# Kernel tuning notes

Measured on AMD Instinct MI355X. Metric: run time of the kernel, lower is better.

The kernel has to match this reference:

```python
import jax, jax.numpy as jnp
import numpy as np

N_NODES = 50000
NUM_FEAT = 2000
HEADS = 8
HID = 8
NUM_CLASSES = 30
NUM_EDGES = 1_600_000
NEG_SLOPE = 0.2


def _segment_softmax(scores, seg, num_segments):
    # scores: [E, H], seg: [E] destination node ids
    m = jax.ops.segment_max(scores, seg, num_segments=num_segments)
    m = jnp.where(jnp.isfinite(m), m, 0.0)  # guard empty segments
    e = jnp.exp(scores - m[seg])
    s = jax.ops.segment_sum(e, seg, num_segments=num_segments)
    return e / (s[seg] + 1e-16)


def _gat_layer(x, src, dst, w, att_src, att_dst, bias, concat):
    # PyG GATConv (eval mode: dropout disabled). x: [N, F_in]
    n = x.shape[0]
    h_, c_ = att_src.shape
    h = (x @ w).reshape(n, h_, c_)                      # [N, H, C]
    a_src = (h * att_src[None]).sum(-1)                 # [N, H]
    a_dst = (h * att_dst[None]).sum(-1)                 # [N, H]
    alpha = jax.nn.leaky_relu(a_src[src] + a_dst[dst], NEG_SLOPE)  # [E, H]
    alpha = _segment_softmax(alpha, dst, n)             # per-dest softmax
    msg = h[src] * alpha[:, :, None]                    # [E, H, C]
    out = jax.ops.segment_sum(msg, dst, num_segments=n) # [N, H, C]
    out = out.reshape(n, h_ * c_) if concat else out.mean(axis=1)
    return out + bias, alpha


def _add_self_loops(edge_index, n):
    loops = jnp.arange(n, dtype=edge_index.dtype)
    src = jnp.concatenate([edge_index[0], loops])
    dst = jnp.concatenate([edge_index[1], loops])
    return src, dst


def setup_inputs() -> dict:
    key = jax.random.key(0)
    ks = jax.random.split(key, 12)
    x = jax.random.normal(ks[0], (N_NODES, NUM_FEAT), jnp.float32)
    edge_index = jax.random.randint(ks[1], (2, NUM_EDGES), 0, N_NODES, jnp.int32)
    d1 = HEADS * HID
    w_res = jax.random.normal(ks[2], (NUM_FEAT, d1), jnp.float32) / np.sqrt(NUM_FEAT)
    b_res = jnp.zeros((d1,), jnp.float32)
    w1 = jax.random.normal(ks[3], (NUM_FEAT, d1), jnp.float32) / np.sqrt(NUM_FEAT)
    att_src1 = jax.random.normal(ks[4], (HEADS, HID), jnp.float32) * 0.1
    att_dst1 = jax.random.normal(ks[5], (HEADS, HID), jnp.float32) * 0.1
    b1 = jnp.zeros((d1,), jnp.float32)
    w2 = jax.random.normal(ks[6], (d1, NUM_CLASSES), jnp.float32) / np.sqrt(d1)
    att_src2 = jax.random.normal(ks[7], (1, NUM_CLASSES), jnp.float32) * 0.1
    att_dst2 = jax.random.normal(ks[8], (1, NUM_CLASSES), jnp.float32) * 0.1
    b2 = jnp.zeros((NUM_CLASSES,), jnp.float32)
    return {"x": x, "edge_index": edge_index, "w_res": w_res, "b_res": b_res,
            "w1": w1, "att_src1": att_src1, "att_dst1": att_dst1, "b1": b1,
            "w2": w2, "att_src2": att_src2, "att_dst2": att_dst2, "b2": b2}


def reference(x, edge_index, w_res, b_res, w1, att_src1, att_dst1, b1,
              w2, att_src2, att_dst2, b2):
    n = x.shape[0]
    src, dst = _add_self_loops(edge_index, n)
    res = x @ w_res + b_res                                   # residual branch
    h1, alpha1 = _gat_layer(x, src, dst, w1, att_src1, att_dst1, b1, concat=True)
    x1 = jax.nn.elu(h1 + res)                                 # dropout = identity (eval)
    h2, alpha2 = _gat_layer(x1, src, dst, w2, att_src2, att_dst2, b2, concat=False)
    x2 = jax.nn.elu(h2)
    return jax.nn.log_softmax(x2, axis=1), alpha1, alpha2
```

## Files before the change

kernel.cpp:

```cpp
#include <hip/hip_runtime.h>
#include <hip/hip_bf16.h>

#define N_NODES 50000
#define NUM_FEAT 2000
#define HEADS 8
#define HID 8
#define NUM_CLASSES 30
#define NUM_EDGES 1600000
#define E_TOTAL (NUM_EDGES + N_NODES)
#define E8 (E_TOTAL * 8)
#define KT32 64
#define KT64 32
#define ROWCAP 128
#define LOG2E 1.44269504f
#define SENT N_NODES
#define NEG_BIG -1.0e30f

typedef __attribute__((ext_vector_type(8))) short short8;
typedef __attribute__((ext_vector_type(4))) float f32x4;

__device__ __forceinline__ ushort f2bf(float f) {
  __hip_bfloat16 b = __float2bfloat16(f);
  return *reinterpret_cast<ushort*>(&b);
}

__device__ __forceinline__ float bf2f(ushort u) {
  unsigned int x = ((unsigned int)u) << 16;
  union { unsigned int i; float f; } c; c.i = x;
  return c.f;
}

__device__ __forceinline__ float lexp2(float sc) {
  return exp2f(fmaxf(sc, 0.2f * sc));
}

__device__ __forceinline__ short8 cvt8(float4 a, float4 b) {
  union { short8 v; ushort u[8]; } p;
  p.u[0] = f2bf(a.x); p.u[1] = f2bf(a.y); p.u[2] = f2bf(a.z); p.u[3] = f2bf(a.w);
  p.u[4] = f2bf(b.x); p.u[5] = f2bf(b.y); p.u[6] = f2bf(b.z); p.u[7] = f2bf(b.w);
  return p.v;
}

__global__ void k_prepB(const float* __restrict__ Wres, const float* __restrict__ W1,
                        ushort* __restrict__ Bp) {
  int i = blockIdx.x * 256 + threadIdx.x;
  if (i >= KT32 * 4 * 128) return;
  int col = i & 127;
  int kbase = (i >> 7) * 8;
  const float* W = (col < 64) ? Wres : W1;
  int c = col & 63;
  union { short8 v; ushort u[8]; } p;
#pragma unroll
  for (int j = 0; j < 8; ++j) {
    int k = kbase + j;
    p.u[j] = f2bf(k < NUM_FEAT ? W[(size_t)k * 64 + c] : 0.f);
  }
  *(short8*)&Bp[(size_t)i * 8] = p.v;
}

__global__ __launch_bounds__(256) void k_prefill(int* __restrict__ esrc) {
  int i = blockIdx.x * 256 + threadIdx.x;
  if (i >= N_NODES * ROWCAP / 4) return;
  *(int4*)&esrc[i * 4] = make_int4(SENT, SENT, SENT, SENT);
}

__global__ __launch_bounds__(256) void k_gemm_mfma(const float* __restrict__ X,
    const ushort* __restrict__ Bp, const float* __restrict__ brs,
    const float* __restrict__ b1, float* __restrict__ Hres,
    ushort* __restrict__ Hatt) {
  __shared__ ushort ldsB[2][8192];
  const int tid = threadIdx.x;
  const int lane = tid & 63, wid = tid >> 6;
  const int lg = lane >> 4, lr = lane & 15;
  const int m0 = blockIdx.x * 64;

  int rowg = m0 + wid * 16 + lr;
  rowg = rowg < N_NODES ? rowg : N_NODES - 1;
  const float* axp = X + (size_t)rowg * NUM_FEAT + lg * 8;
  const short8* bsrc = (const short8*)Bp;

  f32x4 acc[8] = {};
  float4 a[4], na[4];
  short8 gb[4];
  const float4 fz = make_float4(0.f, 0.f, 0.f, 0.f);

  auto loadA = [&](int t, float4* r) {
#pragma unroll
    for (int s = 0; s < 2; ++s) {
      int k0 = t * 64 + s * 32 + lg * 8;
      if (k0 < NUM_FEAT) {
        r[2 * s]     = *(const float4*)(axp + t * 64 + s * 32);
        r[2 * s + 1] = *(const float4*)(axp + t * 64 + s * 32 + 4);
      } else { r[2 * s] = fz; r[2 * s + 1] = fz; }
    }
  };
  auto loadB = [&](int t) {
#pragma unroll
    for (int q = 0; q < 4; ++q) gb[q] = bsrc[(size_t)t * 1024 + q * 256 + tid];
  };
  auto writeB = [&](int buf) {
#pragma unroll
    for (int q = 0; q < 4; ++q)
      *(short8*)&ldsB[buf][(size_t)(q * 256 + tid) * 8] = gb[q];
  };
  auto mfmaStep = [&](int cur, const float4* av) {
#pragma unroll
    for (int s = 0; s < 2; ++s) {
      short8 fb[8];
#pragma unroll
      for (int n = 0; n < 8; ++n)
        fb[n] = *(const short8*)&ldsB[cur][(size_t)(s * 512 + lg * 128 + n * 16 + lr) * 8];
      short8 fa = cvt8(av[2 * s], av[2 * s + 1]);
#pragma unroll
      for (int n = 0; n < 8; ++n)
        acc[n] = __builtin_amdgcn_mfma_f32_16x16x32_bf16(fa, fb[n], acc[n], 0, 0, 0);
    }
  };

  loadB(0);
  loadA(0, a);
  writeB(0);
  asm volatile("s_waitcnt lgkmcnt(0)" ::: "memory");
  __builtin_amdgcn_s_barrier();
  __builtin_amdgcn_sched_barrier(0);

  for (int t = 0; t < KT64 - 1; ++t) {
    const int cur = t & 1, nxt = cur ^ 1;
    loadB(t + 1);
    loadA(t + 1, na);
    mfmaStep(cur, a);
    writeB(nxt);
    asm volatile("s_waitcnt lgkmcnt(0)" ::: "memory");
    __builtin_amdgcn_s_barrier();
    __builtin_amdgcn_sched_barrier(0);
#pragma unroll
    for (int q = 0; q < 4; ++q) a[q] = na[q];
  }
  mfmaStep((KT64 - 1) & 1, a);

#pragma unroll
  for (int n = 0; n < 8; ++n) {
    int col = n * 16 + lr;
    if (col < 64) {
      float badd = brs[col] + b1[col];
#pragma unroll
      for (int i = 0; i < 4; ++i) {
        int row = m0 + wid * 16 + lg * 4 + i;
        if (row < N_NODES) Hres[(size_t)row * 64 + col] = acc[n][i] + badd;
      }
    } else {
#pragma unroll
      for (int i = 0; i < 4; ++i) {
        int row = m0 + wid * 16 + lg * 4 + i;
        if (row < N_NODES) Hatt[(size_t)row * 64 + (col - 64)] = f2bf(acc[n][i]);
      }
    }
  }
}

__global__ void k_fill_attn(const int* __restrict__ ei, int* __restrict__ cursor,
                            int* __restrict__ esrc, ushort* __restrict__ Hatt,
                            const float* __restrict__ att_src,
                            const float* __restrict__ att_dst,
                            float* __restrict__ a_src, float2* __restrict__ dinv1) {
  int i = blockIdx.x * 256 + threadIdx.x;
  if (i < N_NODES * HEADS) {
    int h = i & 7;
    const ushort* hp = &Hatt[(size_t)(i >> 3) * 64 + h * 8];
    float s = 0.f, d = 0.f;
#pragma unroll
    for (int c = 0; c < 8; ++c) {
      float v = bf2f(hp[c]);
      s = fmaf(v, att_src[h * 8 + c], s);
      d = fmaf(v, att_dst[h * 8 + c], d);
    }
    a_src[i] = s * LOG2E;
    dinv1[i] = make_float2(d * LOG2E, 0.f);
  }
  if (i < E_TOTAL) {
    int s, d;
    if (i < NUM_EDGES) { s = ei[i]; d = ei[NUM_EDGES + i]; }
    else { s = d = i - NUM_EDGES; }
    int pos = atomicAdd(&cursor[d], 1);
    esrc[(unsigned)(d * ROWCAP + pos)] = s;
  }
  if (i < 64) Hatt[(size_t)SENT * 64 + i] = 0;
  if (i >= 64 && i < 72) a_src[SENT * 8 + (i - 64)] = NEG_BIG;
}

__global__ __launch_bounds__(256) void k_layer1f(const int* __restrict__ esrc,
    const int* __restrict__ cursor,
    const float* __restrict__ Hres, const ushort* __restrict__ Hatt,
    const float* __restrict__ a_src, float2* __restrict__ dinv1,
    const float* __restrict__ w2, const float* __restrict__ att_src2,
    const float* __restrict__ att_dst2, ushort* __restrict__ h2b,
    float* __restrict__ a_src2, float2* __restrict__ dinv2) {
  __shared__ float w2s[64 * 30];
  __shared__ float xs[4][64];
  for (int i = threadIdx.x; i < 64 * 30; i += 256) w2s[i] = w2[i];
  if (blockIdx.x == 0) {
    if (threadIdx.x < 32) h2b[(unsigned)(SENT * 32 + threadIdx.x)] = 0;
    if (threadIdx.x == 32) a_src2[SENT] = NEG_BIG;
  }
  __syncthreads();
  int wave = threadIdx.x >> 6, lane = threadIdx.x & 63;
  int n = blockIdx.x * 4 + wave;
  if (n >= N_NODES) return;
  int hd = lane >> 3;
  float adn = dinv1[(unsigned)(n * 8 + hd)].x;
  int start = n * ROWCAP, end = start + ((cursor[n] + 7) & ~7);
  float denom = 0.f, msg = 0.f;
  for (int p = start; p < end; p += 8) {
    int4 v0 = *(const int4*)&esrc[p];
    int4 v1 = *(const int4*)&esrc[p + 4];
    int s8[8] = {v0.x, v0.y, v0.z, v0.w, v1.x, v1.y, v1.z, v1.w};
    float av[8];
    ushort hu[8];
#pragma unroll
    for (int i = 0; i < 8; ++i) {
      av[i] = a_src[(unsigned)(s8[i] * 8 + hd)];
      hu[i] = Hatt[(unsigned)(s8[i] * 64 + lane)];
    }
#pragma unroll
    for (int i = 0; i < 8; ++i) {
      float ev = lexp2(av[i] + adn);
      denom += ev;
      msg = fmaf(ev, bf2f(hu[i]), msg);
    }
  }
  float invd = 1.f / (denom + 1e-16f);
  float x1v = msg * invd + Hres[(unsigned)(n * 64 + lane)];
  x1v = x1v > 0.f ? x1v : __expf(x1v) - 1.f;
  if ((lane & 7) == 0) dinv1[(unsigned)(n * 8 + hd)].y = invd;

  xs[wave][lane] = x1v;
  float acc2 = 0.f;
  if (lane < 30) {
#pragma unroll 8
    for (int k = 0; k < 64; ++k) acc2 = fmaf(xs[wave][k], w2s[k * 30 + lane], acc2);
  }
  float as = (lane < 30) ? acc2 * att_src2[lane] : 0.f;
  float ad = (lane < 30) ? acc2 * att_dst2[lane] : 0.f;
  for (int off = 1; off < 64; off <<= 1) {
    as += __shfl_xor(as, off);
    ad += __shfl_xor(ad, off);
  }
  if (lane == 0) { a_src2[n] = as * LOG2E; dinv2[n] = make_float2(ad * LOG2E, 0.f); }
  if (lane < 32) h2b[(unsigned)(n * 32 + lane)] = (lane < 30) ? f2bf(acc2) : (ushort)0;
}

__global__ __launch_bounds__(256) void k_layer2(const int* __restrict__ esrc,
    const int* __restrict__ cursor,
    const ushort* __restrict__ h2b, const float* __restrict__ a_src2,
    float2* __restrict__ dinv2, const float* __restrict__ b2,
    float* __restrict__ out0) {
  int wave = threadIdx.x >> 6, lane = threadIdx.x & 63;
  int n = blockIdx.x * 4 + wave;
  if (n >= N_NODES) return;
  float adn = dinv2[n].x;
  int start = n * ROWCAP, end = start + ((cursor[n] + 7) & ~7);
  int half = lane >> 5, cls = lane & 31;
  float denom = 0.f, msg = 0.f;
  for (int p = start; p < end; p += 4) {
    int s0 = esrc[p + half];
    int s1 = esrc[p + 2 + half];
    float as0 = a_src2[(unsigned)s0], as1 = a_src2[(unsigned)s1];
    ushort hv0 = h2b[(unsigned)(s0 * 32 + cls)];
    ushort hv1 = h2b[(unsigned)(s1 * 32 + cls)];
    float ev0 = lexp2(as0 + adn);
    denom += ev0;
    msg = fmaf(ev0, bf2f(hv0), msg);
    float ev1 = lexp2(as1 + adn);
    denom += ev1;
    msg = fmaf(ev1, bf2f(hv1), msg);
  }
  denom += __shfl_xor(denom, 32);
  msg   += __shfl_xor(msg, 32);
  float invd = 1.f / (denom + 1e-16f);
  bool act = lane < 30;
  float o = act ? msg * invd + b2[lane] : 0.f;
  float x2 = o > 0.f ? o : __expf(o) - 1.f;
  float mv = act ? x2 : -1e30f;
  for (int off = 1; off < 64; off <<= 1) mv = fmaxf(mv, __shfl_xor(mv, off));
  float ex = act ? __expf(x2 - mv) : 0.f;
  for (int off = 1; off < 64; off <<= 1) ex += __shfl_xor(ex, off);
  if (act) out0[(size_t)n * 30 + lane] = x2 - mv - __logf(ex);
  if (lane == 0) dinv2[n].y = invd;
}

__global__ __launch_bounds__(256) void k_alpha(const int* __restrict__ ei,
    const float* __restrict__ a_src1, const float2* __restrict__ dinv1,
    const float* __restrict__ a_src2, const float2* __restrict__ dinv2,
    float* __restrict__ alpha1, float* __restrict__ alpha2) {
  int i = blockIdx.x * 256 + threadIdx.x;
  if (i >= E8) return;
  {
    int e = i >> 3, h = i & 7;
    int s, d;
    if (e < NUM_EDGES) { s = ei[e]; d = ei[NUM_EDGES + e]; }
    else { s = d = e - NUM_EDGES; }
    float2 di = dinv1[(unsigned)(d * 8 + h)];
    alpha1[i] = lexp2(a_src1[(unsigned)(s * 8 + h)] + di.x) * di.y;
  }
  if (i < E_TOTAL) {
    int s, d;
    if (i < NUM_EDGES) { s = ei[i]; d = ei[NUM_EDGES + i]; }
    else { s = d = i - NUM_EDGES; }
    float2 dj = dinv2[(unsigned)d];
    alpha2[i] = lexp2(a_src2[(unsigned)s] + dj.x) * dj.y;
  }
}

extern "C" void kernel_launch(void* const* d_in, const int* in_sizes, int n_in,
                              void* d_out, int out_size, void* d_ws, size_t ws_size,
                              hipStream_t stream) {
  const float* x        = (const float*)d_in[0];
  const int*   ei       = (const int*)d_in[1];
  const float* w_res    = (const float*)d_in[2];
  const float* b_res    = (const float*)d_in[3];
  const float* w1       = (const float*)d_in[4];
  const float* att_src1 = (const float*)d_in[5];
  const float* att_dst1 = (const float*)d_in[6];
  const float* b1       = (const float*)d_in[7];
  const float* w2       = (const float*)d_in[8];
  const float* att_src2 = (const float*)d_in[9];
  const float* att_dst2 = (const float*)d_in[10];
  const float* b2       = (const float*)d_in[11];

  float* ws = (float*)d_ws;
  float* Hres    = ws;
  float* a_src1  = Hres + (size_t)N_NODES * 64;
  float2* dinv1  = (float2*)(a_src1 + (size_t)(N_NODES + 1) * 8);
  float* a_src2  = (float*)(dinv1 + (size_t)N_NODES * 8);
  float2* dinv2  = (float2*)(a_src2 + N_NODES + 1);
  ushort* Hatt   = (ushort*)(dinv2 + N_NODES);
  ushort* h2b    = Hatt + (size_t)(N_NODES + 1) * 64;
  ushort* Bp     = h2b + (size_t)(N_NODES + 1) * 32 + 32;
  int*   cursor  = (int*)(Bp + (size_t)KT32 * 4096 + 64);

  float* out0   = (float*)d_out;
  float* alpha1 = out0 + (size_t)N_NODES * 30;
  float* alpha2 = alpha1 + (size_t)E8;
  int*   esrc   = (int*)alpha1;

  hipMemsetAsync(cursor, 0, N_NODES * sizeof(int), stream);

  k_prefill<<<(N_NODES * ROWCAP / 4 + 255) / 256, 256, 0, stream>>>(esrc);
  k_prepB<<<(KT32 * 4 * 128 + 255) / 256, 256, 0, stream>>>(w_res, w1, Bp);
  k_gemm_mfma<<<(N_NODES + 63) / 64, 256, 0, stream>>>(x, Bp, b_res, b1, Hres, Hatt);
  k_fill_attn<<<(E_TOTAL + 255) / 256, 256, 0, stream>>>(ei, cursor, esrc, Hatt,
                                                         att_src1, att_dst1,
                                                         a_src1, dinv1);
  k_layer1f<<<(N_NODES + 3) / 4, 256, 0, stream>>>(esrc, cursor, Hres, Hatt,
                                                   a_src1, dinv1, w2, att_src2,
                                                   att_dst2, h2b, a_src2, dinv2);
  k_layer2<<<(N_NODES + 3) / 4, 256, 0, stream>>>(esrc, cursor, h2b, a_src2,
                                                  dinv2, b2, out0);
  k_alpha<<<(E8 + 255) / 256, 256, 0, stream>>>(ei, a_src1, dinv1, a_src2, dinv2,
                                                alpha1, alpha2);
}
```

Measured before the change: 436.4 us.

## Load GEMM B tiles directly into LDS and fuse init kernels

The GEMM now stages the bf16 weight tiles with global_load_lds (direct global-to-LDS DMA) instead of loading into registers and writing to LDS, and waits on vmcnt rather than lgkmcnt before the barrier. This removes the register round-trip and the LDS store instructions from the main loop, which frees VGPRs and issue slots. Separately, the memset, the sentinel prefill and the weight-packing kernels are merged into one init kernel to cut launch overhead. The vmcnt(4) wait has to count outstanding loads correctly. If the compiler reorders the A loads and the DMA, the barrier could read stale LDS.

```diff
diff --git a/kernel.cpp b/kernel.cpp
--- a/kernel.cpp
+++ b/kernel.cpp
@@ -19,6 +19,13 @@
 typedef __attribute__((ext_vector_type(8))) short short8;
 typedef __attribute__((ext_vector_type(4))) float f32x4;
 
+typedef __attribute__((address_space(1))) const unsigned int gu32;
+typedef __attribute__((address_space(3))) unsigned int lu32;
+
+__device__ __forceinline__ void gload_lds16(const void* g, void* l) {
+  __builtin_amdgcn_global_load_lds((gu32*)g, (lu32*)l, 16, 0, 0);
+}
+
 __device__ __forceinline__ ushort f2bf(float f) {
   __hip_bfloat16 b = __float2bfloat16(f);
   return *reinterpret_cast<ushort*>(&b);
@@ -41,27 +48,27 @@
   return p.v;
 }
 
-__global__ void k_prepB(const float* __restrict__ Wres, const float* __restrict__ W1,
-                        ushort* __restrict__ Bp) {
+__global__ __launch_bounds__(256) void k_init(int* __restrict__ esrc,
+    const float* __restrict__ Wres, const float* __restrict__ W1,
+    ushort* __restrict__ Bp, int* __restrict__ cursor) {
   int i = blockIdx.x * 256 + threadIdx.x;
-  if (i >= KT32 * 4 * 128) return;
-  int col = i & 127;
-  int kbase = (i >> 7) * 8;
-  const float* W = (col < 64) ? Wres : W1;
-  int c = col & 63;
-  union { short8 v; ushort u[8]; } p;
-#pragma unroll
-  for (int j = 0; j < 8; ++j) {
-    int k = kbase + j;
-    p.u[j] = f2bf(k < NUM_FEAT ? W[(size_t)k * 64 + c] : 0.f);
-  }
-  *(short8*)&Bp[(size_t)i * 8] = p.v;
-}
-
-__global__ __launch_bounds__(256) void k_prefill(int* __restrict__ esrc) {
-  int i = blockIdx.x * 256 + threadIdx.x;
-  if (i >= N_NODES * ROWCAP / 4) return;
-  *(int4*)&esrc[i * 4] = make_int4(SENT, SENT, SENT, SENT);
+  if (i < N_NODES * ROWCAP / 4)
+    *(int4*)&esrc[i * 4] = make_int4(SENT, SENT, SENT, SENT);
+  if (i < N_NODES / 4)
+    *(int4*)&cursor[i * 4] = make_int4(0, 0, 0, 0);
+  if (i < KT32 * 4 * 128) {
+    int col = i & 127;
+    int kbase = (i >> 7) * 8;
+    const float* W = (col < 64) ? Wres : W1;
+    int c = col & 63;
+    union { short8 v; ushort u[8]; } p;
+#pragma unroll
+    for (int j = 0; j < 8; ++j) {
+      int k = kbase + j;
+      p.u[j] = f2bf(k < NUM_FEAT ? W[(size_t)k * 64 + c] : 0.f);
+    }
+    *(short8*)&Bp[(size_t)i * 8] = p.v;
+  }
 }
 
 __global__ __launch_bounds__(256) void k_gemm_mfma(const float* __restrict__ X,
@@ -77,11 +84,9 @@
   int rowg = m0 + wid * 16 + lr;
   rowg = rowg < N_NODES ? rowg : N_NODES - 1;
   const float* axp = X + (size_t)rowg * NUM_FEAT + lg * 8;
-  const short8* bsrc = (const short8*)Bp;
 
   f32x4 acc[8] = {};
   float4 a[4], na[4];
-  short8 gb[4];
   const float4 fz = make_float4(0.f, 0.f, 0.f, 0.f);
 
   auto loadA = [&](int t, float4* r) {
@@ -94,14 +99,12 @@
       } else { r[2 * s] = fz; r[2 * s + 1] = fz; }
     }
   };
-  auto loadB = [&](int t) {
-#pragma unroll
-    for (int q = 0; q < 4; ++q) gb[q] = bsrc[(size_t)t * 1024 + q * 256 + tid];
-  };
-  auto writeB = [&](int buf) {
-#pragma unroll
-    for (int q = 0; q < 4; ++q)
-      *(short8*)&ldsB[buf][(size_t)(q * 256 + tid) * 8] = gb[q];
+  auto dmaB = [&](int t, int buf) {
+#pragma unroll
+    for (int q = 0; q < 4; ++q) {
+      const ushort* g = Bp + ((size_t)t * 1024 + q * 256 + wid * 64 + lane) * 8;
+      gload_lds16(g, &ldsB[buf][(size_t)(q * 256 + wid * 64) * 8]);
+    }
   };
   auto mfmaStep = [&](int cur, const float4* av) {
 #pragma unroll
@@ -117,20 +120,20 @@
     }
   };
 
-  loadB(0);
+  dmaB(0, 0);
+  __builtin_amdgcn_sched_barrier(0);
   loadA(0, a);
-  writeB(0);
-  asm volatile("s_waitcnt lgkmcnt(0)" ::: "memory");
+  asm volatile("s_waitcnt vmcnt(4)" ::: "memory");
   __builtin_amdgcn_s_barrier();
   __builtin_amdgcn_sched_barrier(0);
 
   for (int t = 0; t < KT64 - 1; ++t) {
     const int cur = t & 1, nxt = cur ^ 1;
-    loadB(t + 1);
+    dmaB(t + 1, nxt);
+    __builtin_amdgcn_sched_barrier(0);
     loadA(t + 1, na);
     mfmaStep(cur, a);
-    writeB(nxt);
-    asm volatile("s_waitcnt lgkmcnt(0)" ::: "memory");
+    asm volatile("s_waitcnt vmcnt(4)" ::: "memory");
     __builtin_amdgcn_s_barrier();
     __builtin_amdgcn_sched_barrier(0);
 #pragma unroll
@@ -343,10 +346,8 @@
   float* alpha2 = alpha1 + (size_t)E8;
   int*   esrc   = (int*)alpha1;
 
-  hipMemsetAsync(cursor, 0, N_NODES * sizeof(int), stream);
-
-  k_prefill<<<(N_NODES * ROWCAP / 4 + 255) / 256, 256, 0, stream>>>(esrc);
-  k_prepB<<<(KT32 * 4 * 128 + 255) / 256, 256, 0, stream>>>(w_res, w1, Bp);
+  k_init<<<(N_NODES * ROWCAP / 4 + 255) / 256, 256, 0, stream>>>(esrc, w_res, w1,
+                                                                 Bp, cursor);
   k_gemm_mfma<<<(N_NODES + 63) / 64, 256, 0, stream>>>(x, Bp, b_res, b1, Hres, Hatt);
   k_fill_attn<<<(E_TOTAL + 255) / 256, 256, 0, stream>>>(ei, cursor, esrc, Hatt,
                                                          att_src1, att_dst1,
```

New measurement: 432.0 us. About the same (-1.0%).
